# Kernel optimization log

Hardware: AMD Instinct MI355X
Metric: run time of the kernel (lower is better)

Reference implementation:

```python
import jax, jax.numpy as jnp
import numpy as np

EPS = 1e-6          # module eps for denominator
KERNEL_EPS = 1e-4   # performer softmax_kernel numerical eps


def softmax_kernel(data, projection):
    # data: [n, l, h, e]; projection: [m, e] -> features [n, l, h, m]
    d = data.shape[-1]
    m = projection.shape[0]
    data_normalizer = d ** -0.25
    ratio = m ** -0.5
    data_dash = jnp.einsum('nlhe,me->nlhm', data * data_normalizer, projection)
    diag_data = (0.5 * (data_normalizer ** 2)) * jnp.sum(data * data, axis=-1, keepdims=True)
    # numerically stable exp with per-row max subtraction
    data_dash = ratio * (jnp.exp(data_dash - diag_data - jnp.max(data_dash, axis=-1, keepdims=True)) + KERNEL_EPS)
    return data_dash


def _gaussian_orthogonal_random_matrix(nb_rows, nb_cols, seed=0):
    rng = np.random.default_rng(seed)
    blocks = []
    for _ in range(int(np.ceil(nb_rows / nb_cols))):
        q, _ = np.linalg.qr(rng.standard_normal((nb_cols, nb_cols)))
        blocks.append(q.T)
    proj = np.concatenate(blocks, axis=0)[:nb_rows]
    # scaling=0: chi-distributed row multipliers
    multiplier = np.linalg.norm(rng.standard_normal((nb_rows, nb_cols)), axis=1)
    return (multiplier[:, None] * proj).astype(np.float32)


def setup_inputs() -> dict:
    n, l, h, e = 2, 2048, 8, 64
    nb_features = l  # module: nb_features = l when l >= e
    key = jax.random.key(0)
    kq, kk, kv = jax.random.split(key, 3)
    queries = jax.random.normal(kq, (n, l, h, e), jnp.float32)
    keys = jax.random.normal(kk, (n, l, h, e), jnp.float32)
    values = jax.random.normal(kv, (n, l, h, e), jnp.float32)
    projection = jnp.asarray(_gaussian_orthogonal_random_matrix(nb_features, e))
    return {"queries": queries, "keys": keys, "values": values, "projection": projection}


def reference(queries, keys, values, projection):
    # Performer linear attention, batched (bi=None) branch
    q = softmax_kernel(queries, projection)   # [n, l, h, m]
    k = softmax_kernel(keys, projection)      # [n, l, h, m]
    kv = jnp.einsum('nshm,nshe->nhem', k, values)              # [n, h, e, m]
    z = 1.0 / (jnp.einsum('nlhm,nhm->nlh', q, k.sum(axis=1)) + EPS)  # [n, l, h]
    v = jnp.einsum('nlhm,nhem,nlh->nlhe', q, kv, z)             # [n, l, h, e]
    return v
```

## Files before the change

### kernel.cpp

```cpp
#include <hip/hip_runtime.h>


#define LL 2048
#define HH 8
#define MM 2048
#define ROWSTR 512

#define NORMC 0.35355339059327373f
#define LOG2E 1.4426950408889634f
#define NORMC2 (NORMC * LOG2E)
#define RATIO 0.022097086912079608f
#define KEPS 1e-4f
#define REPS (RATIO * KEPS)
#define EPSD 1e-6f

#define KVSPLIT 2097152
#define RSPLIT 32768

typedef __attribute__((ext_vector_type(8))) short short8;
typedef __attribute__((ext_vector_type(16))) float f32x16;

#define MFMA32(a, b, c) __builtin_amdgcn_mfma_f32_32x32x16_bf16((a), (b), (c), 0, 0, 0)

__device__ __forceinline__ void wg_barrier_lds() {
    asm volatile("s_waitcnt lgkmcnt(0)" ::: "memory");
    __builtin_amdgcn_s_barrier();
    __builtin_amdgcn_sched_barrier(0);
}

__device__ __forceinline__ f32x16 zero16() {
    f32x16 v;
    #pragma unroll
    for (int i = 0; i < 16; ++i) v[i] = 0.f;
    return v;
}
__device__ __forceinline__ unsigned short f2bf(float f) {
    union { float f; unsigned int u; } v; v.f = f;
    unsigned int r = v.u + 0x7fffu + ((v.u >> 16) & 1u);
    return (unsigned short)(r >> 16);
}
__device__ __forceinline__ unsigned int pk2(float lo, float hi) {
    return __builtin_amdgcn_perm(__float_as_uint(hi), __float_as_uint(lo), 0x07060302u);
}
__device__ __forceinline__ float bf2f(unsigned short u) {
    union { unsigned int ui; float f; } v; v.ui = ((unsigned int)u) << 16; return v.f;
}

template <bool BF16>
__device__ __forceinline__ void tile_load(const void* src, size_t base, size_t rstride,
                                          int t, uint4& A, uint4& B) {
    const int row = t >> 2, c16 = (t & 3) * 16;
    if (BF16) {
        const unsigned short* p = (const unsigned short*)src + base + (size_t)row * rstride + c16;
        A = *(const uint4*)p;
        B = *(const uint4*)(p + 8);
    } else {
        const float* p = (const float*)src + base + (size_t)row * rstride + c16;
        float4 f0 = ((const float4*)p)[0], f1 = ((const float4*)p)[1];
        float4 f2 = ((const float4*)p)[2], f3 = ((const float4*)p)[3];
        A.x = pk2(f0.x, f0.y); A.y = pk2(f0.z, f0.w);
        A.z = pk2(f1.x, f1.y); A.w = pk2(f1.z, f1.w);
        B.x = pk2(f2.x, f2.y); B.y = pk2(f2.z, f2.w);
        B.z = pk2(f3.x, f3.y); B.w = pk2(f3.z, f3.w);
    }
}
__device__ __forceinline__ void tile_store72(unsigned short* D, int t, uint4 A, uint4 B) {
    const int row = t >> 2, c16 = (t & 3) * 16;
    *(uint4*)&D[row * 72 + c16] = A;
    *(uint4*)&D[row * 72 + c16 + 8] = B;
}

template <bool BF16>
__device__ __forceinline__ void vt_load(const void* V, size_t base, int t, uint4& A, uint4& B) {
    const int s0 = (t & 31) * 2, e0 = (t >> 5) * 8;
    if (BF16) {
        const unsigned short* p = (const unsigned short*)V + base + (size_t)s0 * ROWSTR + e0;
        A = *(const uint4*)p;
        B = *(const uint4*)(p + ROWSTR);
    } else {
        const float* p = (const float*)V + base + (size_t)s0 * ROWSTR + e0;
        float4 f0 = ((const float4*)p)[0], f1 = ((const float4*)p)[1];
        const float* q = p + ROWSTR;
        float4 g0 = ((const float4*)q)[0], g1 = ((const float4*)q)[1];
        A.x = pk2(f0.x, f0.y); A.y = pk2(f0.z, f0.w);
        A.z = pk2(f1.x, f1.y); A.w = pk2(f1.z, f1.w);
        B.x = pk2(g0.x, g0.y); B.y = pk2(g0.z, g0.w);
        B.z = pk2(g1.x, g1.y); B.w = pk2(g1.z, g1.w);
    }
}
__device__ __forceinline__ void vt_store72(unsigned short* VT, int t, uint4 A, uint4 B) {
    const int s0 = (t & 31) * 2, e0 = (t >> 5) * 8;
    const unsigned ua[4] = {A.x, A.y, A.z, A.w}, ub[4] = {B.x, B.y, B.z, B.w};
    #pragma unroll
    for (int i = 0; i < 4; ++i) {
        *(unsigned*)&VT[(e0 + 2 * i) * 72 + s0] = (ua[i] & 0xFFFFu) | (ub[i] << 16);
        *(unsigned*)&VT[(e0 + 2 * i + 1) * 72 + s0] = (ua[i] >> 16) | (ub[i] & 0xFFFF0000u);
    }
}

__device__ __forceinline__ short8 xfrag(const unsigned int pd[8], int cp, int hi) {
    const unsigned int s0 = hi ? pd[4 * cp + 0] : pd[4 * cp + 2];
    const unsigned int s1 = hi ? pd[4 * cp + 1] : pd[4 * cp + 3];
    const unsigned int r0 = (unsigned int)__shfl_xor((int)s0, 32);
    const unsigned int r1 = (unsigned int)__shfl_xor((int)s1, 32);
    union { unsigned int u[4]; short8 s; } v;
    v.u[0] = hi ? r0 : pd[4 * cp + 0];
    v.u[1] = hi ? r1 : pd[4 * cp + 1];
    v.u[2] = hi ? pd[4 * cp + 2] : r0;
    v.u[3] = hi ? pd[4 * cp + 3] : r1;
    return v.s;
}

__global__ void LinearAttention_15985868276494_detect(const unsigned short* __restrict__ P,
                                                      float* __restrict__ flag) {
    if (threadIdx.x == 0) {
        int sane = 1;
        #pragma unroll
        for (int i = 0; i < 16; ++i) {
            const unsigned e = (P[2 * i] >> 7) & 0xFF;
            if (e < 101 || e > 141) sane = 0;
        }
        *flag = sane ? 1.0f : 0.0f;
    }
}

template <bool BF16>
__device__ void stats_impl(const void* X, const void* P, float* cws,
                           unsigned short* Xs, unsigned short* Ps, float* red) {
    const int t = threadIdx.x;
    const int w = t >> 6, ln = t & 31, hi = (t >> 5) & 1;
    const int rstrip = w & 1, mstrip = w >> 1;
    const int row_base = blockIdx.x * 64;

    uint4 a0, b0;
    tile_load<BF16>(X, (size_t)row_base * 64, 64, t, a0, b0);
    tile_store72(Xs, t, a0, b0);
    tile_load<BF16>(P, 0, 64, t, a0, b0);
    tile_store72(Ps, t, a0, b0);
    uint4 pA, pB;
    tile_load<BF16>(P, (size_t)64 * 64, 64, t, pA, pB);
    wg_barrier_lds();

    short8 xb[4];
    #pragma unroll
    for (int c = 0; c < 4; ++c)
        xb[c] = *(const short8*)&Xs[(32 * rstrip + ln) * 72 + 16 * c + 8 * hi];

    float rmax = -3e38f;
    for (int i = 0; i < 32; ++i) {
        const int cur = i & 1;
        unsigned short* Pc = Ps + cur * 4608;
        f32x16 acc = zero16();
        #pragma unroll
        for (int c = 0; c < 4; ++c) {
            const short8 af = *(const short8*)&Pc[(32 * mstrip + ln) * 72 + 16 * c + 8 * hi];
            acc = MFMA32(af, xb[c], acc);
        }
        if (i + 1 < 32) {
            tile_store72(Ps + (cur ^ 1) * 4608, t, pA, pB);
            if (i + 2 < 32)
                tile_load<BF16>(P, (size_t)((i + 2) * 64) * 64, 64, t, pA, pB);
        }
        #pragma unroll
        for (int r = 0; r < 16; ++r) rmax = fmaxf(rmax, acc[r]);
        wg_barrier_lds();
    }
    rmax = fmaxf(rmax, __shfl_xor(rmax, 32));
    if (hi == 0) red[w * 32 + ln] = rmax;
    wg_barrier_lds();
    if (t < 64) {
        const int rs = t >> 5;
        const float rm = fmaxf(red[rs * 32 + (t & 31)], red[(rs + 2) * 32 + (t & 31)]);
        float s2 = 0.f;
        #pragma unroll
        for (int c = 0; c < 64; c += 8) {
            uint4 u = *(const uint4*)&Xs[t * 72 + c];
            const unsigned int ua[4] = {u.x, u.y, u.z, u.w};
            #pragma unroll
            for (int i = 0; i < 4; ++i) {
                const float lo = bf2f((unsigned short)(ua[i] & 0xFFFF));
                const float hv = bf2f((unsigned short)(ua[i] >> 16));
                s2 = fmaf(lo, lo, s2); s2 = fmaf(hv, hv, s2);
            }
        }
        const int rg = row_base + t;
        const int n = rg >> 14, l = (rg >> 3) & 2047, h = rg & 7;
        cws[(size_t)((n << 3) | h) * LL + l] =
            (NORMC * rm + (0.5f * NORMC * NORMC) * s2) * LOG2E;
    }
}

__global__ __launch_bounds__(256, 4) void LinearAttention_15985868276494_stats(
        const void* K, const void* Q, const void* P, const float* flag,
        float* c_k, float* c_q) {
    __shared__ unsigned short Xs[64 * 72];
    __shared__ unsigned short Ps[2 * 64 * 72];
    __shared__ float red[128];
    const void* X = (blockIdx.y == 0) ? K : Q;
    float* cws = (blockIdx.y == 0) ? c_k : c_q;
    if (*flag != 0.f) stats_impl<true>(X, P, cws, Xs, Ps, red);
    else stats_impl<false>(X, P, cws, Xs, Ps, red);
}

template <bool BF16>
__device__ void kv_impl(const void* K, const void* V, const void* P, const float* cws,
                        float* kvf01, float* ksum01, char* smem) {
    unsigned short* Ks = (unsigned short*)smem;
    unsigned short* VT = (unsigned short*)(smem + 18432);
    float* cks = (float*)(smem + 36864);
    float* fin = (float*)smem;

    const int t = threadIdx.x;
    const int w = t >> 6, ln = t & 31, hi = (t >> 5) & 1;
    const int sstrip = w & 1, mstrip = w >> 1;
    const int bid = blockIdx.x;
    const int xcd = bid & 7, rr = bid >> 3;
    const int ghi = rr & 3, mt = rr >> 2;
    const int g = (ghi << 3) | xcd;
    const int nh = g >> 1, sp = g & 1;
    const int n = nh >> 3, h = nh & 7;
    const size_t xbase = (size_t)n * (LL * ROWSTR) + (size_t)h * 64;
    const int st0 = sp * 16;

    unsigned short* Ps = Ks + 4608;
    {
        uint4 pa, pbv;
        tile_load<BF16>(P, (size_t)(mt * 64) * 64, 64, t, pa, pbv);
        tile_store72(Ps, t, pa, pbv);
    }
    uint4 kA, kB, vA, vB; float ckr = 0.f;
    tile_load<BF16>(K, xbase + (size_t)(st0 * 64) * ROWSTR, ROWSTR, t, kA, kB);
    vt_load<BF16>(V, xbase + (size_t)(st0 * 64) * ROWSTR, t, vA, vB);
    if (t < 64) ckr = cws[(size_t)nh * LL + st0 * 64 + t];
    tile_store72(Ks, t, kA, kB);
    vt_store72(VT, t, vA, vB);
    if (t < 64) cks[t] = ckr;
    tile_load<BF16>(K, xbase + (size_t)((st0 + 1) * 64) * ROWSTR, ROWSTR, t, kA, kB);
    vt_load<BF16>(V, xbase + (size_t)((st0 + 1) * 64) * ROWSTR, t, vA, vB);
    if (t < 64) ckr = cws[(size_t)nh * LL + (st0 + 1) * 64 + t];
    wg_barrier_lds();

    short8 pb[4];
    #pragma unroll
    for (int c = 0; c < 4; ++c)
        pb[c] = *(const short8*)&Ps[(32 * mstrip + ln) * 72 + 16 * c + 8 * hi];
    wg_barrier_lds();
    const short8 ones = {0x3F80, 0x3F80, 0x3F80, 0x3F80, 0x3F80, 0x3F80, 0x3F80, 0x3F80};

    f32x16 akv0 = zero16(), akv1 = zero16(), aks = zero16();

    for (int i = 0; i < 16; ++i) {
        const int cur = i & 1;
        unsigned short* Kc = Ks + cur * 4608;
        unsigned short* Vc = VT + cur * 4608;
        const float* cc = cks + cur * 64;
        f32x16 D = zero16();
        #pragma unroll
        for (int c = 0; c < 4; ++c) {
            const short8 af = *(const short8*)&Kc[(32 * sstrip + ln) * 72 + 16 * c + 8 * hi];
            D = MFMA32(af, pb[c], D);
        }
        if (i + 1 < 16) {
            tile_store72(Ks + (cur ^ 1) * 4608, t, kA, kB);
            vt_store72(VT + (cur ^ 1) * 4608, t, vA, vB);
            if (t < 64) cks[(cur ^ 1) * 64 + t] = ckr;
            if (i + 2 < 16) {
                const int st = st0 + i + 2;
                tile_load<BF16>(K, xbase + (size_t)(st * 64) * ROWSTR, ROWSTR, t, kA, kB);
                vt_load<BF16>(V, xbase + (size_t)(st * 64) * ROWSTR, t, vA, vB);
                if (t < 64) ckr = cws[(size_t)nh * LL + st * 64 + t];
            }
        }
        unsigned int pd[8];
        #pragma unroll
        for (int gIdx = 0; gIdx < 4; ++gIdx) {
            const float4 c4 = *(const float4*)&cc[32 * sstrip + 8 * gIdx + 4 * hi];
            const float ca[4] = {c4.x, c4.y, c4.z, c4.w};
            float f[4];
            #pragma unroll
            for (int b = 0; b < 4; ++b) {
                const float arg = fminf(fmaf(D[4 * gIdx + b], NORMC2, -ca[b]), 0.f);
                f[b] = fmaf(__builtin_amdgcn_exp2f(arg), RATIO, REPS);
            }
            pd[2 * gIdx] = pk2(f[0], f[1]);
            pd[2 * gIdx + 1] = pk2(f[2], f[3]);
        }
        #pragma unroll
        for (int cp = 0; cp < 2; ++cp) {
            const short8 bf = xfrag(pd, cp, hi);
            const int scol = 32 * sstrip + 16 * cp + 8 * hi;
            const short8 v0 = *(const short8*)&Vc[ln * 72 + scol];
            const short8 v1 = *(const short8*)&Vc[(32 + ln) * 72 + scol];
            akv0 = MFMA32(v0, bf, akv0);
            akv1 = MFMA32(v1, bf, akv1);
            aks = MFMA32(ones, bf, aks);
        }
        wg_barrier_lds();
    }
    {
        const int slot = (w * 64 + (t & 63)) * 33;
        #pragma unroll
        for (int r = 0; r < 16; ++r) fin[slot + r] = akv0[r];
        #pragma unroll
        for (int r = 0; r < 16; ++r) fin[slot + 16 + r] = akv1[r];
        fin[slot + 32] = aks[0];
    }
    wg_barrier_lds();
    {
        const int e = t >> 2;
        const int t16 = e >> 5, e5 = e & 31;
        const int hi_s = (e5 >> 2) & 1;
        const int reg = 16 * t16 + (e5 & 3) + 4 * (e5 >> 3);
        float* dst = kvf01 + (size_t)sp * KVSPLIT + (size_t)nh * (64 * MM)
                   + (size_t)e * MM + mt * 64 + (t & 3) * 16;
        #pragma unroll
        for (int jq = 0; jq < 4; ++jq) {
            float o[4];
            #pragma unroll
            for (int b = 0; b < 4; ++b) {
                const int m_local = (t & 3) * 16 + 4 * jq + b;
                const int ms = m_local >> 5;
                const int lane_s = hi_s * 32 + (m_local & 31);
                o[b] = fin[((2 * ms) * 64 + lane_s) * 33 + reg]
                     + fin[((2 * ms + 1) * 64 + lane_s) * 33 + reg];
            }
            *(float4*)&dst[4 * jq] = make_float4(o[0], o[1], o[2], o[3]);
        }
        if (t < 64) {
            const int ms = t >> 5;
            const float val = fin[((2 * ms) * 64 + (t & 31)) * 33 + 32]
                            + fin[((2 * ms + 1) * 64 + (t & 31)) * 33 + 32];
            ksum01[(size_t)sp * RSPLIT + (size_t)nh * MM + mt * 64 + t] = val;
        }
    }
}

__global__ __launch_bounds__(256, 4) void LinearAttention_15985868276494_kv(
        const void* K, const void* V, const void* P, const float* flag,
        const float* cws, float* kvf01, float* ksum01) {
    extern __shared__ char smem_kv[];
    if (*flag != 0.f) kv_impl<true>(K, V, P, cws, kvf01, ksum01, smem_kv);
    else kv_impl<false>(K, V, P, cws, kvf01, ksum01, smem_kv);
}

__global__ __launch_bounds__(256) void LinearAttention_15985868276494_reduce(
        const float* __restrict__ kvf01, const float* __restrict__ ksum01,
        unsigned short* __restrict__ kvT, float* __restrict__ ksumW) {
    const int gid = blockIdx.x * 256 + threadIdx.x;
    const size_t i4 = (size_t)gid * 4;
    const float4 a = *(const float4*)&kvf01[i4];
    const float4 b = *(const float4*)&kvf01[KVSPLIT + i4];
    uint2 o;
    o.x = (unsigned)f2bf(a.x + b.x) | ((unsigned)f2bf(a.y + b.y) << 16);
    o.y = (unsigned)f2bf(a.z + b.z) | ((unsigned)f2bf(a.w + b.w) << 16);
    *(uint2*)&kvT[i4] = o;
    if (blockIdx.x < 32) {
        const float4 c = *(const float4*)&ksum01[i4];
        const float4 d = *(const float4*)&ksum01[RSPLIT + i4];
        *(float4*)&ksumW[i4] = make_float4(c.x + d.x, c.y + d.y, c.z + d.z, c.w + d.w);
    }
}

template <bool BF16>
__device__ void out_impl(const void* Q, const void* P, const float* cqw,
                         const unsigned short* kvT, const float* ksum,
                         float* po, float* pad, char* smem) {
    unsigned short* Ps = (unsigned short*)smem;
    unsigned short* KVs = (unsigned short*)(smem + 18432);
    unsigned short* kss = (unsigned short*)(smem + 36864);
    float* fin = (float*)smem;

    const int t = threadIdx.x;
    const int w = t >> 6, ln = t & 31, hi = (t >> 5) & 1;
    const int mstrip = w & 1, lstrip = w >> 1;
    const int bid = blockIdx.x;
    const int xcd = bid & 7, rr = bid >> 3;
    const int ghi = rr & 3, lb = rr >> 2;
    const int g = (ghi << 3) | xcd;
    const int nh = g >> 1, sp = g & 1;
    const int n = nh >> 3, h = nh & 7;
    const size_t qbase = (size_t)n * (LL * ROWSTR) + (size_t)h * 64 + (size_t)(lb * 64) * ROWSTR;
    const size_t kvbase = (size_t)nh * (size_t)(64 * MM);
    const int mt0 = sp * 16;

    unsigned short* Qs = Ps + 4608;
    {
        uint4 qa, qbv;
        tile_load<BF16>(Q, qbase, ROWSTR, t, qa, qbv);
        tile_store72(Qs, t, qa, qbv);
    }
    uint4 pA, pB, kA, kB; float ksr = 0.f;
    tile_load<BF16>(P, (size_t)(mt0 * 64) * 64, 64, t, pA, pB);
    tile_load<true>(kvT, kvbase + mt0 * 64, MM, t, kA, kB);
    if (t < 64) ksr = ksum[(size_t)nh * MM + mt0 * 64 + t];
    tile_store72(Ps, t, pA, pB);
    tile_store72(KVs, t, kA, kB);
    if (t < 64) kss[t] = f2bf(ksr);
    tile_load<BF16>(P, (size_t)((mt0 + 1) * 64) * 64, 64, t, pA, pB);
    tile_load<true>(kvT, kvbase + (mt0 + 1) * 64, MM, t, kA, kB);
    if (t < 64) ksr = ksum[(size_t)nh * MM + (mt0 + 1) * 64 + t];
    wg_barrier_lds();

    short8 qb[4];
    #pragma unroll
    for (int c = 0; c < 4; ++c)
        qb[c] = *(const short8*)&Qs[(32 * lstrip + ln) * 72 + 16 * c + 8 * hi];
    const float cq = cqw[(size_t)nh * LL + lb * 64 + lstrip * 32 + ln];
    wg_barrier_lds();

    f32x16 ao0 = zero16(), ao1 = zero16(), ad = zero16();

    for (int i = 0; i < 16; ++i) {
        const int cur = i & 1;
        unsigned short* Pc = Ps + cur * 4608;
        unsigned short* Kc = KVs + cur * 4608;
        const unsigned short* ksc = kss + cur * 64;
        f32x16 D = zero16();
        #pragma unroll
        for (int c = 0; c < 4; ++c) {
            const short8 af = *(const short8*)&Pc[(32 * mstrip + ln) * 72 + 16 * c + 8 * hi];
            D = MFMA32(af, qb[c], D);
        }
        if (i + 1 < 16) {
            tile_store72(Ps + (cur ^ 1) * 4608, t, pA, pB);
            tile_store72(KVs + (cur ^ 1) * 4608, t, kA, kB);
            if (t < 64) kss[(cur ^ 1) * 64 + t] = f2bf(ksr);
            if (i + 2 < 16) {
                tile_load<BF16>(P, (size_t)((mt0 + i + 2) * 64) * 64, 64, t, pA, pB);
                tile_load<true>(kvT, kvbase + (mt0 + i + 2) * 64, MM, t, kA, kB);
                if (t < 64) ksr = ksum[(size_t)nh * MM + (mt0 + i + 2) * 64 + t];
            }
        }
        unsigned int pd[8];
        #pragma unroll
        for (int gIdx = 0; gIdx < 4; ++gIdx) {
            float f[4];
            #pragma unroll
            for (int b = 0; b < 4; ++b) {
                const float arg = fminf(fmaf(D[4 * gIdx + b], NORMC2, -cq), 0.f);
                f[b] = fmaf(__builtin_amdgcn_exp2f(arg), RATIO, REPS);
            }
            pd[2 * gIdx] = pk2(f[0], f[1]);
            pd[2 * gIdx + 1] = pk2(f[2], f[3]);
        }
        #pragma unroll
        for (int cp = 0; cp < 2; ++cp) {
            const short8 bf = xfrag(pd, cp, hi);
            const int mcol = 32 * mstrip + 16 * cp + 8 * hi;
            const short8 a0 = *(const short8*)&Kc[ln * 72 + mcol];
            const short8 a1 = *(const short8*)&Kc[(32 + ln) * 72 + mcol];
            const short8 k8 = *(const short8*)&ksc[mcol];
            ao0 = MFMA32(a0, bf, ao0);
            ao1 = MFMA32(a1, bf, ao1);
            ad = MFMA32(k8, bf, ad);
        }
        wg_barrier_lds();
    }
    {
        const int slot = (w * 64 + (t & 63)) * 33;
        #pragma unroll
        for (int r = 0; r < 16; ++r) fin[slot + r] = ao0[r];
        #pragma unroll
        for (int r = 0; r < 16; ++r) fin[slot + 16 + r] = ao1[r];
        fin[slot + 32] = ad[0];
    }
    wg_barrier_lds();
    {
        const int l_local = t >> 2, eg = t & 3;
        const int ls = l_local >> 5, lane_l = l_local & 31;
        const float adt = fin[((2 * ls) * 64 + lane_l) * 33 + 32]
                        + fin[((2 * ls + 1) * 64 + lane_l) * 33 + 32];
        const int l = lb * 64 + l_local;
        const size_t row = (size_t)(n * LL + l) * HH + h;
        if (eg == 0) pad[(size_t)sp * RSPLIT + row] = adt;
        float* dst = po + (size_t)sp * KVSPLIT + row * 64 + eg * 16;
        #pragma unroll
        for (int jq = 0; jq < 4; ++jq) {
            float o[4];
            #pragma unroll
            for (int b = 0; b < 4; ++b) {
                const int e = eg * 16 + 4 * jq + b;
                const int t16 = e >> 5, e5 = e & 31;
                const int hi_s = (e5 >> 2) & 1;
                const int reg = 16 * t16 + (e5 & 3) + 4 * (e5 >> 3);
                const int lane_s = hi_s * 32 + lane_l;
                o[b] = fin[((2 * ls) * 64 + lane_s) * 33 + reg]
                     + fin[((2 * ls + 1) * 64 + lane_s) * 33 + reg];
            }
            *(float4*)&dst[4 * jq] = make_float4(o[0], o[1], o[2], o[3]);
        }
    }
}

__global__ __launch_bounds__(256, 4) void LinearAttention_15985868276494_out(
        const void* Q, const void* P, const float* flag, const float* cqw,
        const unsigned short* kvT, const float* ksum, float* po, float* pad) {
    extern __shared__ char smem_out[];
    if (*flag != 0.f) out_impl<true>(Q, P, cqw, kvT, ksum, po, pad, smem_out);
    else out_impl<false>(Q, P, cqw, kvT, ksum, po, pad, smem_out);
}

__global__ __launch_bounds__(256) void LinearAttention_15985868276494_out2(
        const float* __restrict__ po, const float* __restrict__ pad,
        const float* __restrict__ flag, void* __restrict__ outp) {
    const int gid = blockIdx.x * 256 + threadIdx.x;
    const int row = gid >> 2, eg = gid & 3;
    const float adt = pad[row] + pad[RSPLIT + row];
    const float z = 1.0f / (adt + EPSD);
    const size_t base = (size_t)row * 64 + eg * 16;
    float vals[16];
    #pragma unroll
    for (int q4 = 0; q4 < 4; ++q4) {
        const float4 a = *(const float4*)&po[base + 4 * q4];
        const float4 b = *(const float4*)&po[KVSPLIT + base + 4 * q4];
        vals[4 * q4 + 0] = (a.x + b.x) * z;
        vals[4 * q4 + 1] = (a.y + b.y) * z;
        vals[4 * q4 + 2] = (a.z + b.z) * z;
        vals[4 * q4 + 3] = (a.w + b.w) * z;
    }
    if (*flag != 0.f) {
        uint4 o0, o1;
        o0.x = (unsigned)f2bf(vals[0]) | ((unsigned)f2bf(vals[1]) << 16);
        o0.y = (unsigned)f2bf(vals[2]) | ((unsigned)f2bf(vals[3]) << 16);
        o0.z = (unsigned)f2bf(vals[4]) | ((unsigned)f2bf(vals[5]) << 16);
        o0.w = (unsigned)f2bf(vals[6]) | ((unsigned)f2bf(vals[7]) << 16);
        o1.x = (unsigned)f2bf(vals[8]) | ((unsigned)f2bf(vals[9]) << 16);
        o1.y = (unsigned)f2bf(vals[10]) | ((unsigned)f2bf(vals[11]) << 16);
        o1.z = (unsigned)f2bf(vals[12]) | ((unsigned)f2bf(vals[13]) << 16);
        o1.w = (unsigned)f2bf(vals[14]) | ((unsigned)f2bf(vals[15]) << 16);
        unsigned short* op = (unsigned short*)outp + base;
        *(uint4*)op = o0;
        *(uint4*)(op + 8) = o1;
    } else {
        float* op = (float*)outp + base;
        #pragma unroll
        for (int q4 = 0; q4 < 4; ++q4)
            *(float4*)&op[4 * q4] = make_float4(vals[4 * q4], vals[4 * q4 + 1],
                                                vals[4 * q4 + 2], vals[4 * q4 + 3]);
    }
}

extern "C" void kernel_launch(void* const* d_in, const int* in_sizes, int n_in,
                              void* d_out, int out_size, void* d_ws, size_t ws_size,
                              hipStream_t stream) {
    const void* Q = d_in[0];
    const void* K = d_in[1];
    const void* V = d_in[2];
    const void* P = d_in[3];

    float* W = (float*)d_ws;
    float* flag = W;
    float* c_k = W + 16;
    float* c_q = c_k + 32768;
    float* ksum01 = c_q + 32768;
    float* kvf01 = ksum01 + 2 * RSPLIT;
    float* ksumW = kvf01 + 2 * KVSPLIT;
    unsigned short* kvTW = (unsigned short*)(ksumW + RSPLIT);

    LinearAttention_15985868276494_detect<<<1, 64, 0, stream>>>(
        (const unsigned short*)P, flag);
    LinearAttention_15985868276494_stats<<<dim3(512, 2), 256, 0, stream>>>(
        K, Q, P, flag, c_k, c_q);
    LinearAttention_15985868276494_kv<<<dim3(1024), 256, 37376, stream>>>(
        K, V, P, flag, c_k, kvf01, ksum01);
    LinearAttention_15985868276494_reduce<<<2048, 256, 0, stream>>>(
        kvf01, ksum01, kvTW, ksumW);
    LinearAttention_15985868276494_out<<<dim3(1024), 256, 37120, stream>>>(
        Q, P, flag, c_q, kvTW, ksumW, kvf01, ksum01);
    LinearAttention_15985868276494_out2<<<512, 256, 0, stream>>>(
        kvf01, ksum01, flag, d_out);
}
```

Measured before the change: 219.1 us.

## Widen stats/kv/out workgroups to 1024 threads sharing staged LDS tiles

```diff
diff --git a/kernel.cpp b/kernel.cpp
--- a/kernel.cpp
+++ b/kernel.cpp
@@ -44,6 +44,20 @@
 }
 __device__ __forceinline__ float bf2f(unsigned short u) {
     union { unsigned int ui; float f; } v; v.ui = ((unsigned int)u) << 16; return v.f;
+}
+
+template <bool BF16>
+__device__ __forceinline__ short8 row_load8(const void* src, size_t rowbase, int off) {
+    if (BF16) {
+        return *(const short8*)((const unsigned short*)src + rowbase + off);
+    } else {
+        const float* p = (const float*)src + rowbase + off;
+        float4 f0 = ((const float4*)p)[0], f1 = ((const float4*)p)[1];
+        union { unsigned int u[4]; short8 s; } v;
+        v.u[0] = pk2(f0.x, f0.y); v.u[1] = pk2(f0.z, f0.w);
+        v.u[2] = pk2(f1.x, f1.y); v.u[3] = pk2(f1.z, f1.w);
+        return v.s;
+    }
 }
 
 template <bool BF16>
@@ -126,25 +140,27 @@
 
 template <bool BF16>
 __device__ void stats_impl(const void* X, const void* P, float* cws,
-                           unsigned short* Xs, unsigned short* Ps, float* red) {
+                           unsigned short* Ps, float* red) {
     const int t = threadIdx.x;
     const int w = t >> 6, ln = t & 31, hi = (t >> 5) & 1;
-    const int rstrip = w & 1, mstrip = w >> 1;
-    const int row_base = blockIdx.x * 64;
-
-    uint4 a0, b0;
-    tile_load<BF16>(X, (size_t)row_base * 64, 64, t, a0, b0);
-    tile_store72(Xs, t, a0, b0);
-    tile_load<BF16>(P, 0, 64, t, a0, b0);
-    tile_store72(Ps, t, a0, b0);
-    uint4 pA, pB;
-    tile_load<BF16>(P, (size_t)64 * 64, 64, t, pA, pB);
-    wg_barrier_lds();
+    const int mstrip = w & 1, rstrip = w >> 1;
+    const int row_base = blockIdx.x * 256;
 
     short8 xb[4];
     #pragma unroll
     for (int c = 0; c < 4; ++c)
-        xb[c] = *(const short8*)&Xs[(32 * rstrip + ln) * 72 + 16 * c + 8 * hi];
+        xb[c] = row_load8<BF16>(X, (size_t)(row_base + rstrip * 32 + ln) * 64, 16 * c + 8 * hi);
+
+    const bool stP = (t < 256);
+    const int tl = t & 255;
+    uint4 pA, pB;
+    if (stP) {
+        uint4 a0, b0;
+        tile_load<BF16>(P, 0, 64, tl, a0, b0);
+        tile_store72(Ps, tl, a0, b0);
+        tile_load<BF16>(P, (size_t)64 * 64, 64, tl, pA, pB);
+    }
+    wg_barrier_lds();
 
     float rmax = -3e38f;
     for (int i = 0; i < 32; ++i) {
@@ -156,10 +172,10 @@
             const short8 af = *(const short8*)&Pc[(32 * mstrip + ln) * 72 + 16 * c + 8 * hi];
             acc = MFMA32(af, xb[c], acc);
         }
-        if (i + 1 < 32) {
-            tile_store72(Ps + (cur ^ 1) * 4608, t, pA, pB);
+        if (stP && i + 1 < 32) {
+            tile_store72(Ps + (cur ^ 1) * 4608, tl, pA, pB);
             if (i + 2 < 32)
-                tile_load<BF16>(P, (size_t)((i + 2) * 64) * 64, 64, t, pA, pB);
+                tile_load<BF16>(P, (size_t)((i + 2) * 64) * 64, 64, tl, pA, pB);
         }
         #pragma unroll
         for (int r = 0; r < 16; ++r) rmax = fmaxf(rmax, acc[r]);
@@ -167,39 +183,39 @@
     }
     rmax = fmaxf(rmax, __shfl_xor(rmax, 32));
     if (hi == 0) red[w * 32 + ln] = rmax;
+    float s2 = 0.f;
+    if (mstrip == 0) {
+        #pragma unroll
+        for (int c = 0; c < 4; ++c) {
+            union { short8 s; unsigned int u[4]; } uv; uv.s = xb[c];
+            #pragma unroll
+            for (int i2 = 0; i2 < 4; ++i2) {
+                const float lo = bf2f((unsigned short)(uv.u[i2] & 0xFFFF));
+                const float hv = bf2f((unsigned short)(uv.u[i2] >> 16));
+                s2 = fmaf(lo, lo, s2); s2 = fmaf(hv, hv, s2);
+            }
+        }
+        s2 += __shfl_xor(s2, 32);
+    }
     wg_barrier_lds();
-    if (t < 64) {
-        const int rs = t >> 5;
-        const float rm = fmaxf(red[rs * 32 + (t & 31)], red[(rs + 2) * 32 + (t & 31)]);
-        float s2 = 0.f;
-        #pragma unroll
-        for (int c = 0; c < 64; c += 8) {
-            uint4 u = *(const uint4*)&Xs[t * 72 + c];
-            const unsigned int ua[4] = {u.x, u.y, u.z, u.w};
-            #pragma unroll
-            for (int i = 0; i < 4; ++i) {
-                const float lo = bf2f((unsigned short)(ua[i] & 0xFFFF));
-                const float hv = bf2f((unsigned short)(ua[i] >> 16));
-                s2 = fmaf(lo, lo, s2); s2 = fmaf(hv, hv, s2);
-            }
-        }
-        const int rg = row_base + t;
+    if (mstrip == 0 && hi == 0) {
+        const float rm = fmaxf(red[w * 32 + ln], red[(w + 1) * 32 + ln]);
+        const int rg = row_base + rstrip * 32 + ln;
         const int n = rg >> 14, l = (rg >> 3) & 2047, h = rg & 7;
         cws[(size_t)((n << 3) | h) * LL + l] =
             (NORMC * rm + (0.5f * NORMC * NORMC) * s2) * LOG2E;
     }
 }
 
-__global__ __launch_bounds__(256, 4) void LinearAttention_15985868276494_stats(
+__global__ __launch_bounds__(1024, 4) void LinearAttention_15985868276494_stats(
         const void* K, const void* Q, const void* P, const float* flag,
         float* c_k, float* c_q) {
-    __shared__ unsigned short Xs[64 * 72];
     __shared__ unsigned short Ps[2 * 64 * 72];
-    __shared__ float red[128];
+    __shared__ float red[512];
     const void* X = (blockIdx.y == 0) ? K : Q;
     float* cws = (blockIdx.y == 0) ? c_k : c_q;
-    if (*flag != 0.f) stats_impl<true>(X, P, cws, Xs, Ps, red);
-    else stats_impl<false>(X, P, cws, Xs, Ps, red);
+    if (*flag != 0.f) stats_impl<true>(X, P, cws, Ps, red);
+    else stats_impl<false>(X, P, cws, Ps, red);
 }
 
 template <bool BF16>
@@ -212,41 +228,44 @@
 
     const int t = threadIdx.x;
     const int w = t >> 6, ln = t & 31, hi = (t >> 5) & 1;
-    const int sstrip = w & 1, mstrip = w >> 1;
+    const int w2 = w & 3, ep = w >> 2;
+    const int sstrip = w2 & 1, msub = w2 >> 1;
+    const int mc = ep * 2 + msub;
     const int bid = blockIdx.x;
     const int xcd = bid & 7, rr = bid >> 3;
-    const int ghi = rr & 3, mt = rr >> 2;
-    const int g = (ghi << 3) | xcd;
+    const int gq = rr >> 3, mtb = rr & 7;
+    const int g = gq * 8 + xcd;
     const int nh = g >> 1, sp = g & 1;
     const int n = nh >> 3, h = nh & 7;
     const size_t xbase = (size_t)n * (LL * ROWSTR) + (size_t)h * 64;
     const int st0 = sp * 16;
-
-    unsigned short* Ps = Ks + 4608;
-    {
-        uint4 pa, pbv;
-        tile_load<BF16>(P, (size_t)(mt * 64) * 64, 64, t, pa, pbv);
-        tile_store72(Ps, t, pa, pbv);
-    }
-    uint4 kA, kB, vA, vB; float ckr = 0.f;
-    tile_load<BF16>(K, xbase + (size_t)(st0 * 64) * ROWSTR, ROWSTR, t, kA, kB);
-    vt_load<BF16>(V, xbase + (size_t)(st0 * 64) * ROWSTR, t, vA, vB);
-    if (t < 64) ckr = cws[(size_t)nh * LL + st0 * 64 + t];
-    tile_store72(Ks, t, kA, kB);
-    vt_store72(VT, t, vA, vB);
-    if (t < 64) cks[t] = ckr;
-    tile_load<BF16>(K, xbase + (size_t)((st0 + 1) * 64) * ROWSTR, ROWSTR, t, kA, kB);
-    vt_load<BF16>(V, xbase + (size_t)((st0 + 1) * 64) * ROWSTR, t, vA, vB);
-    if (t < 64) ckr = cws[(size_t)nh * LL + (st0 + 1) * 64 + t];
-    wg_barrier_lds();
+    const int mbase = mtb * 256;
+
+    const bool stK = (t < 256), stV = (t >= 256 && t < 512);
+    const int tl = t & 255;
 
     short8 pb[4];
     #pragma unroll
     for (int c = 0; c < 4; ++c)
-        pb[c] = *(const short8*)&Ps[(32 * mstrip + ln) * 72 + 16 * c + 8 * hi];
+        pb[c] = row_load8<BF16>(P, (size_t)(mbase + mc * 32 + ln) * 64, 16 * c + 8 * hi);
+
+    uint4 kA, kB, vA, vB; float ckr = 0.f;
+    if (stK) {
+        tile_load<BF16>(K, xbase + (size_t)(st0 * 64) * ROWSTR, ROWSTR, tl, kA, kB);
+        tile_store72(Ks, tl, kA, kB);
+        tile_load<BF16>(K, xbase + (size_t)((st0 + 1) * 64) * ROWSTR, ROWSTR, tl, kA, kB);
+    } else if (stV) {
+        vt_load<BF16>(V, xbase + (size_t)(st0 * 64) * ROWSTR, tl, vA, vB);
+        vt_store72(VT, tl, vA, vB);
+        vt_load<BF16>(V, xbase + (size_t)((st0 + 1) * 64) * ROWSTR, tl, vA, vB);
+    }
+    if (t < 64) {
+        cks[t] = cws[(size_t)nh * LL + st0 * 64 + t];
+        ckr = cws[(size_t)nh * LL + (st0 + 1) * 64 + t];
+    }
     wg_barrier_lds();
+
     const short8 ones = {0x3F80, 0x3F80, 0x3F80, 0x3F80, 0x3F80, 0x3F80, 0x3F80, 0x3F80};
-
     f32x16 akv0 = zero16(), akv1 = zero16(), aks = zero16();
 
     for (int i = 0; i < 16; ++i) {
@@ -261,13 +280,13 @@
             D = MFMA32(af, pb[c], D);
         }
         if (i + 1 < 16) {
-            tile_store72(Ks + (cur ^ 1) * 4608, t, kA, kB);
-            vt_store72(VT + (cur ^ 1) * 4608, t, vA, vB);
+            if (stK) tile_store72(Ks + (cur ^ 1) * 4608, tl, kA, kB);
+            else if (stV) vt_store72(VT + (cur ^ 1) * 4608, tl, vA, vB);
             if (t < 64) cks[(cur ^ 1) * 64 + t] = ckr;
             if (i + 2 < 16) {
                 const int st = st0 + i + 2;
-                tile_load<BF16>(K, xbase + (size_t)(st * 64) * ROWSTR, ROWSTR, t, kA, kB);
-                vt_load<BF16>(V, xbase + (size_t)(st * 64) * ROWSTR, t, vA, vB);
+                if (stK) tile_load<BF16>(K, xbase + (size_t)(st * 64) * ROWSTR, ROWSTR, tl, kA, kB);
+                else if (stV) vt_load<BF16>(V, xbase + (size_t)(st * 64) * ROWSTR, tl, vA, vB);
                 if (t < 64) ckr = cws[(size_t)nh * LL + st * 64 + t];
             }
         }
@@ -297,45 +316,51 @@
         }
         wg_barrier_lds();
     }
-    {
-        const int slot = (w * 64 + (t & 63)) * 33;
-        #pragma unroll
-        for (int r = 0; r < 16; ++r) fin[slot + r] = akv0[r];
-        #pragma unroll
-        for (int r = 0; r < 16; ++r) fin[slot + 16 + r] = akv1[r];
-        fin[slot + 32] = aks[0];
-    }
-    wg_barrier_lds();
-    {
-        const int e = t >> 2;
-        const int t16 = e >> 5, e5 = e & 31;
-        const int hi_s = (e5 >> 2) & 1;
-        const int reg = 16 * t16 + (e5 & 3) + 4 * (e5 >> 3);
-        float* dst = kvf01 + (size_t)sp * KVSPLIT + (size_t)nh * (64 * MM)
-                   + (size_t)e * MM + mt * 64 + (t & 3) * 16;
-        #pragma unroll
-        for (int jq = 0; jq < 4; ++jq) {
-            float o[4];
-            #pragma unroll
-            for (int b = 0; b < 4; ++b) {
-                const int m_local = (t & 3) * 16 + 4 * jq + b;
-                const int ms = m_local >> 5;
-                const int lane_s = hi_s * 32 + (m_local & 31);
-                o[b] = fin[((2 * ms) * 64 + lane_s) * 33 + reg]
-                     + fin[((2 * ms + 1) * 64 + lane_s) * 33 + reg];
-            }
-            *(float4*)&dst[4 * jq] = make_float4(o[0], o[1], o[2], o[3]);
-        }
-        if (t < 64) {
-            const int ms = t >> 5;
-            const float val = fin[((2 * ms) * 64 + (t & 31)) * 33 + 32]
-                            + fin[((2 * ms + 1) * 64 + (t & 31)) * 33 + 32];
-            ksum01[(size_t)sp * RSPLIT + (size_t)nh * MM + mt * 64 + t] = val;
-        }
-    }
-}
-
-__global__ __launch_bounds__(256, 4) void LinearAttention_15985868276494_kv(
+    #pragma unroll 1
+    for (int e4 = 0; e4 < 4; ++e4) {
+        if (ep == e4) {
+            const int slot = (w2 * 64 + (t & 63)) * 33;
+            #pragma unroll
+            for (int r = 0; r < 16; ++r) fin[slot + r] = akv0[r];
+            #pragma unroll
+            for (int r = 0; r < 16; ++r) fin[slot + 16 + r] = akv1[r];
+            fin[slot + 32] = aks[0];
+        }
+        wg_barrier_lds();
+        if (ep == e4) {
+            const int tt = t & 255;
+            const int mt = mtb * 4 + e4;
+            const int e = tt >> 2;
+            const int t16 = e >> 5, e5 = e & 31;
+            const int hi_s = (e5 >> 2) & 1;
+            const int reg = 16 * t16 + (e5 & 3) + 4 * (e5 >> 3);
+            float* dst = kvf01 + (size_t)sp * KVSPLIT + (size_t)nh * (64 * MM)
+                       + (size_t)e * MM + mt * 64 + (tt & 3) * 16;
+            #pragma unroll
+            for (int jq = 0; jq < 4; ++jq) {
+                float o[4];
+                #pragma unroll
+                for (int b = 0; b < 4; ++b) {
+                    const int m_local = (tt & 3) * 16 + 4 * jq + b;
+                    const int ms = m_local >> 5;
+                    const int lane_s = hi_s * 32 + (m_local & 31);
+                    o[b] = fin[((2 * ms) * 64 + lane_s) * 33 + reg]
+                         + fin[((2 * ms + 1) * 64 + lane_s) * 33 + reg];
+                }
+                *(float4*)&dst[4 * jq] = make_float4(o[0], o[1], o[2], o[3]);
+            }
+            if (tt < 64) {
+                const int ms = tt >> 5;
+                const float val = fin[((2 * ms) * 64 + (tt & 31)) * 33 + 32]
+                                + fin[((2 * ms + 1) * 64 + (tt & 31)) * 33 + 32];
+                ksum01[(size_t)sp * RSPLIT + (size_t)nh * MM + mt * 64 + tt] = val;
+            }
+        }
+        wg_barrier_lds();
+    }
+}
+
+__global__ __launch_bounds__(1024, 4) void LinearAttention_15985868276494_kv(
         const void* K, const void* V, const void* P, const float* flag,
         const float* cws, float* kvf01, float* ksum01) {
     extern __shared__ char smem_kv[];
@@ -372,40 +397,43 @@
 
     const int t = threadIdx.x;
     const int w = t >> 6, ln = t & 31, hi = (t >> 5) & 1;
-    const int mstrip = w & 1, lstrip = w >> 1;
+    const int w2 = w & 3, ep = w >> 2;
+    const int mstrip = w2 & 1, lsub = w2 >> 1;
+    const int lc = ep * 2 + lsub;
     const int bid = blockIdx.x;
     const int xcd = bid & 7, rr = bid >> 3;
-    const int ghi = rr & 3, lb = rr >> 2;
-    const int g = (ghi << 3) | xcd;
+    const int gq = rr >> 3, lbb = rr & 7;
+    const int g = gq * 8 + xcd;
     const int nh = g >> 1, sp = g & 1;
     const int n = nh >> 3, h = nh & 7;
-    const size_t qbase = (size_t)n * (LL * ROWSTR) + (size_t)h * 64 + (size_t)(lb * 64) * ROWSTR;
+    const size_t qbase = (size_t)n * (LL * ROWSTR) + (size_t)h * 64;
     const size_t kvbase = (size_t)nh * (size_t)(64 * MM);
     const int mt0 = sp * 16;
-
-    unsigned short* Qs = Ps + 4608;
-    {
-        uint4 qa, qbv;
-        tile_load<BF16>(Q, qbase, ROWSTR, t, qa, qbv);
-        tile_store72(Qs, t, qa, qbv);
-    }
-    uint4 pA, pB, kA, kB; float ksr = 0.f;
-    tile_load<BF16>(P, (size_t)(mt0 * 64) * 64, 64, t, pA, pB);
-    tile_load<true>(kvT, kvbase + mt0 * 64, MM, t, kA, kB);
-    if (t < 64) ksr = ksum[(size_t)nh * MM + mt0 * 64 + t];
-    tile_store72(Ps, t, pA, pB);
-    tile_store72(KVs, t, kA, kB);
-    if (t < 64) kss[t] = f2bf(ksr);
-    tile_load<BF16>(P, (size_t)((mt0 + 1) * 64) * 64, 64, t, pA, pB);
-    tile_load<true>(kvT, kvbase + (mt0 + 1) * 64, MM, t, kA, kB);
-    if (t < 64) ksr = ksum[(size_t)nh * MM + (mt0 + 1) * 64 + t];
-    wg_barrier_lds();
+    const int lbase = lbb * 256;
+
+    const bool stP = (t < 256), stKV = (t >= 256 && t < 512);
+    const int tl = t & 255;
 
     short8 qb[4];
     #pragma unroll
     for (int c = 0; c < 4; ++c)
-        qb[c] = *(const short8*)&Qs[(32 * lstrip + ln) * 72 + 16 * c + 8 * hi];
-    const float cq = cqw[(size_t)nh * LL + lb * 64 + lstrip * 32 + ln];
+        qb[c] = row_load8<BF16>(Q, qbase + (size_t)(lbase + lc * 32 + ln) * ROWSTR, 16 * c + 8 * hi);
+    const float cq = cqw[(size_t)nh * LL + lbase + lc * 32 + ln];
+
+    uint4 pA, pB, kA, kB; float ksr = 0.f;
+    if (stP) {
+        tile_load<BF16>(P, (size_t)(mt0 * 64) * 64, 64, tl, pA, pB);
+        tile_store72(Ps, tl, pA, pB);
+        tile_load<BF16>(P, (size_t)((mt0 + 1) * 64) * 64, 64, tl, pA, pB);
+    } else if (stKV) {
+        tile_load<true>(kvT, kvbase + mt0 * 64, MM, tl, kA, kB);
+        tile_store72(KVs, tl, kA, kB);
+        tile_load<true>(kvT, kvbase + (mt0 + 1) * 64, MM, tl, kA, kB);
+    }
+    if (t < 64) {
+        kss[t] = f2bf(ksum[(size_t)nh * MM + mt0 * 64 + t]);
+        ksr = ksum[(size_t)nh * MM + (mt0 + 1) * 64 + t];
+    }
     wg_barrier_lds();
 
     f32x16 ao0 = zero16(), ao1 = zero16(), ad = zero16();
@@ -422,12 +450,12 @@
             D = MFMA32(af, qb[c], D);
         }
         if (i + 1 < 16) {
-            tile_store72(Ps + (cur ^ 1) * 4608, t, pA, pB);
-            tile_store72(KVs + (cur ^ 1) * 4608, t, kA, kB);
+            if (stP) tile_store72(Ps + (cur ^ 1) * 4608, tl, pA, pB);
+            else if (stKV) tile_store72(KVs + (cur ^ 1) * 4608, tl, kA, kB);
             if (t < 64) kss[(cur ^ 1) * 64 + t] = f2bf(ksr);
             if (i + 2 < 16) {
-                tile_load<BF16>(P, (size_t)((mt0 + i + 2) * 64) * 64, 64, t, pA, pB);
-                tile_load<true>(kvT, kvbase + (mt0 + i + 2) * 64, MM, t, kA, kB);
+                if (stP) tile_load<BF16>(P, (size_t)((mt0 + i + 2) * 64) * 64, 64, tl, pA, pB);
+                else if (stKV) tile_load<true>(kvT, kvbase + (mt0 + i + 2) * 64, MM, tl, kA, kB);
                 if (t < 64) ksr = ksum[(size_t)nh * MM + (mt0 + i + 2) * 64 + t];
             }
         }
@@ -456,43 +484,48 @@
         }
         wg_barrier_lds();
     }
-    {
-        const int slot = (w * 64 + (t & 63)) * 33;
-        #pragma unroll
-        for (int r = 0; r < 16; ++r) fin[slot + r] = ao0[r];
-        #pragma unroll
-        for (int r = 0; r < 16; ++r) fin[slot + 16 + r] = ao1[r];
-        fin[slot + 32] = ad[0];
-    }
-    wg_barrier_lds();
-    {
-        const int l_local = t >> 2, eg = t & 3;
-        const int ls = l_local >> 5, lane_l = l_local & 31;
-        const float adt = fin[((2 * ls) * 64 + lane_l) * 33 + 32]
-                        + fin[((2 * ls + 1) * 64 + lane_l) * 33 + 32];
-        const int l = lb * 64 + l_local;
-        const size_t row = (size_t)(n * LL + l) * HH + h;
-        if (eg == 0) pad[(size_t)sp * RSPLIT + row] = adt;
-        float* dst = po + (size_t)sp * KVSPLIT + row * 64 + eg * 16;
-        #pragma unroll
-        for (int jq = 0; jq < 4; ++jq) {
-            float o[4];
-            #pragma unroll
-            for (int b = 0; b < 4; ++b) {
-                const int e = eg * 16 + 4 * jq + b;
-                const int t16 = e >> 5, e5 = e & 31;
-                const int hi_s = (e5 >> 2) & 1;
-                const int reg = 16 * t16 + (e5 & 3) + 4 * (e5 >> 3);
-                const int lane_s = hi_s * 32 + lane_l;
-                o[b] = fin[((2 * ls) * 64 + lane_s) * 33 + reg]
-                     + fin[((2 * ls + 1) * 64 + lane_s) * 33 + reg];
-            }
-            *(float4*)&dst[4 * jq] = make_float4(o[0], o[1], o[2], o[3]);
-        }
-    }
-}
-
-__global__ __launch_bounds__(256, 4) void LinearAttention_15985868276494_out(
+    #pragma unroll 1
+    for (int e4 = 0; e4 < 4; ++e4) {
+        if (ep == e4) {
+            const int slot = (w2 * 64 + (t & 63)) * 33;
+            #pragma unroll
+            for (int r = 0; r < 16; ++r) fin[slot + r] = ao0[r];
+            #pragma unroll
+            for (int r = 0; r < 16; ++r) fin[slot + 16 + r] = ao1[r];
+            fin[slot + 32] = ad[0];
+        }
+        wg_barrier_lds();
+        if (ep == e4) {
+            const int tt = t & 255;
+            const int l_local = tt >> 2, eg = tt & 3;
+            const int ls = l_local >> 5, lane_l = l_local & 31;
+            const float adt = fin[((2 * ls) * 64 + lane_l) * 33 + 32]
+                            + fin[((2 * ls + 1) * 64 + lane_l) * 33 + 32];
+            const int l = (lbb * 4 + e4) * 64 + l_local;
+            const size_t row = (size_t)(n * LL + l) * HH + h;
+            if (eg == 0) pad[(size_t)sp * RSPLIT + row] = adt;
+            float* dst = po + (size_t)sp * KVSPLIT + row * 64 + eg * 16;
+            #pragma unroll
+            for (int jq = 0; jq < 4; ++jq) {
+                float o[4];
+                #pragma unroll
+                for (int b = 0; b < 4; ++b) {
+                    const int e = eg * 16 + 4 * jq + b;
+                    const int t16 = e >> 5, e5 = e & 31;
+                    const int hi_s = (e5 >> 2) & 1;
+                    const int reg = 16 * t16 + (e5 & 3) + 4 * (e5 >> 3);
+                    const int lane_s = hi_s * 32 + lane_l;
+                    o[b] = fin[((2 * ls) * 64 + lane_s) * 33 + reg]
+                         + fin[((2 * ls + 1) * 64 + lane_s) * 33 + reg];
+                }
+                *(float4*)&dst[4 * jq] = make_float4(o[0], o[1], o[2], o[3]);
+            }
+        }
+        wg_barrier_lds();
+    }
+}
+
+__global__ __launch_bounds__(1024, 4) void LinearAttention_15985868276494_out(
         const void* Q, const void* P, const float* flag, const float* cqw,
         const unsigned short* kvT, const float* ksum, float* po, float* pad) {
     extern __shared__ char smem_out[];
@@ -559,13 +592,13 @@
 
     LinearAttention_15985868276494_detect<<<1, 64, 0, stream>>>(
         (const unsigned short*)P, flag);
-    LinearAttention_15985868276494_stats<<<dim3(512, 2), 256, 0, stream>>>(
+    LinearAttention_15985868276494_stats<<<dim3(128, 2), 1024, 0, stream>>>(
         K, Q, P, flag, c_k, c_q);
-    LinearAttention_15985868276494_kv<<<dim3(1024), 256, 37376, stream>>>(
+    LinearAttention_15985868276494_kv<<<dim3(256), 1024, 37376, stream>>>(
         K, V, P, flag, c_k, kvf01, ksum01);
     LinearAttention_15985868276494_reduce<<<2048, 256, 0, stream>>>(
         kvf01, ksum01, kvTW, ksumW);
-    LinearAttention_15985868276494_out<<<dim3(1024), 256, 37120, stream>>>(
+    LinearAttention_15985868276494_out<<<dim3(256), 1024, 37120, stream>>>(
         Q, P, flag, c_q, kvTW, ksumW, kvf01, ksum01);
     LinearAttention_15985868276494_out2<<<512, 256, 0, stream>>>(
         kvf01, ksum01, flag, d_out);
```

New measurement: 186.1 us. 1.18x faster.
